# Optimization experiments

Measured on AMD Instinct MI355X. Metric: run time of the kernel, lower is better.

## Reference

```python
import jax, jax.numpy as jnp
import numpy as np

SR = 10  # self.sr in the torch module

def _linear_params(key, fan_in, fan_out):
    kw, kb = jax.random.split(key)
    bound = 1.0 / np.sqrt(fan_in)
    W = jax.random.uniform(kw, (fan_out, fan_in), jnp.float32, -bound, bound)
    b = jax.random.uniform(kb, (fan_out,), jnp.float32, -bound, bound)
    return W, b

def setup_inputs() -> dict:
    key = jax.random.key(0)
    ks = jax.random.split(key, 6)
    P, H = 2048, 1024
    R = C = P * SR
    X = jax.random.normal(ks[0], (R, C), jnp.float32)
    p = jax.random.randint(ks[1], (P,), 0, 64, jnp.int32)
    W1, b1 = _linear_params(ks[2], 1, H)
    W2, b2 = _linear_params(ks[3], H, H)
    W3, b3 = _linear_params(ks[4], H, H)
    W4, b4 = _linear_params(ks[5], H, 1)
    return {"X": X, "p": p, "W1": W1, "b1": b1, "W2": W2, "b2": b2,
            "W3": W3, "b3": b3, "W4": W4, "b4": b4}

def _forward(X, p, W1, b1, W2, b2, W3, b3, W4, b4):
    P = p.shape[0]
    C = X.shape[1]
    # shift_rows: only rows i*SR for i in [0, P-2] are populated; all other
    # rows of the shifted matrix are NaN and contribute 0 sum / 0 count below.
    rows = X[jnp.arange(P - 1) * SR]                      # (P-1, C)
    shifts = p[: P - 1]
    # torch.roll(x, s): out[j] = x[(j - s) mod C]
    cols = (jnp.arange(C)[None, :] - shifts[:, None]) % C  # (P-1, C)
    shifted = jnp.take_along_axis(rows, cols, axis=1)      # (P-1, C)
    # nan_mean over rows (NaN rows of the full matrix drop out identically)
    mask = jnp.isnan(shifted)
    col_sum = jnp.where(mask, 0.0, shifted).sum(axis=0)
    col_cnt = (~mask).sum(axis=0).astype(jnp.float32)
    m = jnp.where(col_cnt > 0, col_sum / col_cnt, jnp.float32(jnp.nan))  # (C,)
    # fill_nan_with_last_value: serial forward-fill (index 0 kept as-is)
    def step(last, xi):
        v = jnp.where(jnp.isnan(xi), last, xi)
        return v, v
    _, rest = jax.lax.scan(step, m[0], m[1:])
    filled = jnp.concatenate([m[:1], rest])                # (C,)
    x = filled[::SR][:P][:, None]                          # (P, 1)
    h = jax.nn.relu(x @ W1.T + b1)
    h = jax.nn.relu(h @ W2.T + b2)
    h = jax.nn.relu(h @ W3.T + b3)
    y = h @ W4.T + b4                                      # (P, 1)
    return y[:, 0]

def reference(X, p, W1, b1, W2, b2, W3, b3, W4, b4):
    return _forward(X, p, W1, b1, W2, b2, W3, b3, W4, b4)
```

## Files before the change

### kernel.cpp

```cpp
#include <hip/hip_runtime.h>
#include <hip/hip_bf16.h>

#define CC 20480
#define PP 2048
#define NROWS 2047
#define SRR 10
#define HH 1024
#define NCH 64

typedef __attribute__((ext_vector_type(8))) short short8;
typedef __attribute__((ext_vector_type(4))) float f32x4;

__device__ __forceinline__ void split_bf16(float v, unsigned short& hi, unsigned short& lo) {
    __hip_bfloat16 h = __float2bfloat16(v);
    float r = v - __bfloat162float(h);
    __hip_bfloat16 l2 = __float2bfloat16(r);
    hi = *(unsigned short*)&h;
    lo = *(unsigned short*)&l2;
}

__global__ __launch_bounds__(256) void pre_k(const float* __restrict__ X,
                                             const int* __restrict__ p,
                                             float* __restrict__ psum,
                                             const float* __restrict__ W2,
                                             unsigned short* __restrict__ w2h,
                                             unsigned short* __restrict__ w2l,
                                             const float* __restrict__ W3,
                                             unsigned short* __restrict__ w3h,
                                             unsigned short* __restrict__ w3l) {
    int b = blockIdx.x, t = threadIdx.x;
    if (b < 512) {
        int k = (b & 7) * 256 + t;
        int chunk = b >> 3;
        int r0 = chunk * 32;
        int r1 = r0 + 32; if (r1 > NROWS) r1 = NROWS;
        float s = 0.f;
        int base = SRR * k;
        for (int i = r0; i < r1; ++i) {
            int col = base - p[i]; if (col < 0) col += CC;
            s += X[(size_t)i * (size_t)(SRR * CC) + col];
        }
        psum[chunk * PP + k] = s;
        return;
    }
    int bb = b - 512;
    const float* src; unsigned short *dh, *dl;
    if (bb < 256) { src = W2; dh = w2h; dl = w2l; }
    else { src = W3; dh = w3h; dl = w3l; bb -= 256; }
    int idx = bb * 4096 + t * 16;
    #pragma unroll
    for (int q = 0; q < 4; ++q) {
        float4 v = *(const float4*)&src[idx + q * 4];
        float vv[4] = {v.x, v.y, v.z, v.w};
        ushort hi4[4], lo4[4];
        #pragma unroll
        for (int i = 0; i < 4; ++i) split_bf16(vv[i], hi4[i], lo4[i]);
        *(ushort4*)&dh[idx + q * 4] = *(ushort4*)hi4;
        *(ushort4*)&dl[idx + q * 4] = *(ushort4*)lo4;
    }
}

__device__ __forceinline__ void gload16(const unsigned short* g, unsigned short* lds) {
    __builtin_amdgcn_global_load_lds(
        (const __attribute__((address_space(1))) void*)g,
        (__attribute__((address_space(3))) void*)lds,
        16, 0, 0);
}

#define BM 128
#define BN 64
#define BK 32

__global__ __launch_bounds__(512, 2) void gemm1_k(
    const float* __restrict__ psum,
    const float* __restrict__ W1, const float* __restrict__ b1,
    const unsigned short* __restrict__ Bh, const unsigned short* __restrict__ Bl,
    const float* __restrict__ b2,
    unsigned short* __restrict__ Ch, unsigned short* __restrict__ Cl)
{
    __shared__ unsigned short Bb[2][4096];
    __shared__ float w1f[1024], b1f[1024], xv[128];

    int lin = blockIdx.x;
    int v = (lin & 7) * 32 + (lin >> 3);
    int bx = v >> 4, by = v & 15;
    int bm = bx * BM, bn = by * BN;
    int t = threadIdx.x, w = t >> 6, l = t & 63;
    int lr = l & 15, lk = l >> 4;
    int wr = w >> 1, wc = w & 1;

    size_t offB = (size_t)(bn + (w & 3) * 16 + lr) * HH + lk * 8;
#define BSTAGE(buf, k0)                                                      \
    do {                                                                     \
        if (w < 4) gload16(Bh + offB + (k0), Bb[buf] + w * 512);             \
        else       gload16(Bl + offB + (k0), Bb[buf] + 2048 + (w - 4) * 512);\
    } while (0)

    BSTAGE(0, 0);
    {
        int row = t >> 2, q = t & 3;
        float s = 0.f;
        #pragma unroll
        for (int j = 0; j < 16; ++j) s += psum[(q * 16 + j) * PP + bm + row];
        s += __shfl_xor(s, 1, 64);
        s += __shfl_xor(s, 2, 64);
        if (q == 0) xv[row] = s * (1.0f / (float)NROWS);
        if (t < 256) *(float4*)&w1f[t * 4] = *(const float4*)&W1[t * 4];
        else *(float4*)&b1f[(t - 256) * 4] = *(const float4*)&b1[(t - 256) * 4];
    }
    __syncthreads();

    float x0 = xv[wr * 32 + lr], x1 = xv[wr * 32 + 16 + lr];

    f32x4 acc[2][2];
    #pragma unroll
    for (int i = 0; i < 2; ++i)
        #pragma unroll
        for (int j = 0; j < 2; ++j) acc[i][j] = (f32x4)(0.f);

    int nt = HH / BK;
    for (int tt = 0; tt < nt; ++tt) {
        int cur = tt & 1;
        if (tt + 1 < nt) {
            BSTAGE(cur ^ 1, (tt + 1) * BK);
            asm volatile("s_waitcnt vmcnt(1)" ::: "memory");
        } else {
            asm volatile("s_waitcnt vmcnt(0)" ::: "memory");
        }
        __builtin_amdgcn_s_barrier();
        __builtin_amdgcn_sched_barrier(0);
        __builtin_amdgcn_s_setprio(1);
        int k0 = tt * BK;
        float4 wva = *(const float4*)&w1f[k0 + lk * 8];
        float4 wvb = *(const float4*)&w1f[k0 + lk * 8 + 4];
        float4 bva = *(const float4*)&b1f[k0 + lk * 8];
        float4 bvb = *(const float4*)&b1f[k0 + lk * 8 + 4];
        float wv[8] = {wva.x, wva.y, wva.z, wva.w, wvb.x, wvb.y, wvb.z, wvb.w};
        float bv2[8] = {bva.x, bva.y, bva.z, bva.w, bvb.x, bvb.y, bvb.z, bvb.w};
        ushort ahh[2][8], all2[2][8];
        #pragma unroll
        for (int mi = 0; mi < 2; ++mi) {
            float xm = mi ? x1 : x0;
            #pragma unroll
            for (int j = 0; j < 8; ++j) {
                float h = fmaf(xm, wv[j], bv2[j]);
                h = h > 0.f ? h : 0.f;
                split_bf16(h, ahh[mi][j], all2[mi][j]);
            }
        }
        short8 bh2[2], bl2[2];
        #pragma unroll
        for (int ni = 0; ni < 2; ++ni) {
            bh2[ni] = *(const short8*)&Bb[cur][(wc * 2 + ni) * 512 + l * 8];
            bl2[ni] = *(const short8*)&Bb[cur][2048 + (wc * 2 + ni) * 512 + l * 8];
        }
        #pragma unroll
        for (int mi = 0; mi < 2; ++mi) {
            short8 ah2 = *(short8*)ahh[mi];
            short8 al2 = *(short8*)all2[mi];
            #pragma unroll
            for (int ni = 0; ni < 2; ++ni) {
                acc[mi][ni] = __builtin_amdgcn_mfma_f32_16x16x32_bf16(ah2, bh2[ni], acc[mi][ni], 0, 0, 0);
                acc[mi][ni] = __builtin_amdgcn_mfma_f32_16x16x32_bf16(ah2, bl2[ni], acc[mi][ni], 0, 0, 0);
                acc[mi][ni] = __builtin_amdgcn_mfma_f32_16x16x32_bf16(al2, bh2[ni], acc[mi][ni], 0, 0, 0);
            }
        }
        __builtin_amdgcn_s_setprio(0);
        __builtin_amdgcn_sched_barrier(0);
        __builtin_amdgcn_s_barrier();
        __builtin_amdgcn_sched_barrier(0);
    }
#undef BSTAGE

    float bv[2];
    #pragma unroll
    for (int ni = 0; ni < 2; ++ni) bv[ni] = b2[bn + wc * 32 + ni * 16 + lr];
    #pragma unroll
    for (int mi = 0; mi < 2; ++mi)
        #pragma unroll
        for (int ni = 0; ni < 2; ++ni)
            #pragma unroll
            for (int r = 0; r < 4; ++r) {
                int row = bm + wr * 32 + mi * 16 + lk * 4 + r;
                int col = bn + wc * 32 + ni * 16 + lr;
                float vv = acc[mi][ni][r] + bv[ni];
                vv = vv > 0.f ? vv : 0.f;
                unsigned short hi, lo;
                split_bf16(vv, hi, lo);
                Ch[(size_t)row * HH + col] = hi;
                Cl[(size_t)row * HH + col] = lo;
            }
}

__global__ __launch_bounds__(512, 2) void gemm2_k(
    const unsigned short* __restrict__ Ah, const unsigned short* __restrict__ Al,
    const unsigned short* __restrict__ Bh, const unsigned short* __restrict__ Bl,
    const float* __restrict__ b3,
    const float* __restrict__ W4, float* __restrict__ partial)
{
    __shared__ unsigned short lds[2][12288];
    int lin = blockIdx.x;
    int v = (lin & 7) * 32 + (lin >> 3);
    int bx = v >> 4, by = v & 15;
    int bm = bx * BM, bn = by * BN;
    int t = threadIdx.x, w = t >> 6, l = t & 63;
    int lr = l & 15, lk = l >> 4;
    int wr = w >> 1, wc = w & 1;

    size_t offA = (size_t)(bm + w * 16 + lr) * HH + lk * 8;
    size_t offB = (size_t)(bn + (w & 3) * 16 + lr) * HH + lk * 8;

#define STAGE(buf, k0)                                                   \
    do {                                                                 \
        unsigned short* L = lds[buf];                                    \
        gload16(Ah + offA + (k0), L + w * 512);                          \
        gload16(Al + offA + (k0), L + 4096 + w * 512);                   \
        if (w < 4) gload16(Bh + offB + (k0), L + 8192 + w * 512);        \
        else       gload16(Bl + offB + (k0), L + 10240 + (w - 4) * 512); \
    } while (0)

    f32x4 acc[2][2];
    #pragma unroll
    for (int i = 0; i < 2; ++i)
        #pragma unroll
        for (int j = 0; j < 2; ++j) acc[i][j] = (f32x4)(0.f);

    STAGE(0, 0);

    int nt = HH / BK;
    for (int tt = 0; tt < nt; ++tt) {
        int cur = tt & 1;
        if (tt + 1 < nt) {
            STAGE(cur ^ 1, (tt + 1) * BK);
            asm volatile("s_waitcnt vmcnt(3)" ::: "memory");
        } else {
            asm volatile("s_waitcnt vmcnt(0)" ::: "memory");
        }
        __builtin_amdgcn_s_barrier();
        __builtin_amdgcn_sched_barrier(0);
        __builtin_amdgcn_s_setprio(1);
        unsigned short* L = lds[cur];
        short8 ah2[2], al2[2], bh2[2], bl2[2];
        #pragma unroll
        for (int mi = 0; mi < 2; ++mi) {
            ah2[mi] = *(const short8*)&L[(wr * 2 + mi) * 512 + l * 8];
            al2[mi] = *(const short8*)&L[4096 + (wr * 2 + mi) * 512 + l * 8];
        }
        #pragma unroll
        for (int ni = 0; ni < 2; ++ni) {
            bh2[ni] = *(const short8*)&L[8192 + (wc * 2 + ni) * 512 + l * 8];
            bl2[ni] = *(const short8*)&L[10240 + (wc * 2 + ni) * 512 + l * 8];
        }
        #pragma unroll
        for (int mi = 0; mi < 2; ++mi)
            #pragma unroll
            for (int ni = 0; ni < 2; ++ni) {
                acc[mi][ni] = __builtin_amdgcn_mfma_f32_16x16x32_bf16(ah2[mi], bh2[ni], acc[mi][ni], 0, 0, 0);
                acc[mi][ni] = __builtin_amdgcn_mfma_f32_16x16x32_bf16(ah2[mi], bl2[ni], acc[mi][ni], 0, 0, 0);
                acc[mi][ni] = __builtin_amdgcn_mfma_f32_16x16x32_bf16(al2[mi], bh2[ni], acc[mi][ni], 0, 0, 0);
            }
        __builtin_amdgcn_s_setprio(0);
        __builtin_amdgcn_sched_barrier(0);
        __builtin_amdgcn_s_barrier();
        __builtin_amdgcn_sched_barrier(0);
    }
#undef STAGE

    float bv[2], w4v[2];
    #pragma unroll
    for (int ni = 0; ni < 2; ++ni) {
        bv[ni]  = b3[bn + wc * 32 + ni * 16 + lr];
        w4v[ni] = W4[bn + wc * 32 + ni * 16 + lr];
    }
    #pragma unroll
    for (int mi = 0; mi < 2; ++mi) {
        float ps[4];
        #pragma unroll
        for (int r = 0; r < 4; ++r) {
            float acc_d = 0.f;
            #pragma unroll
            for (int ni = 0; ni < 2; ++ni) {
                float vv = acc[mi][ni][r] + bv[ni];
                vv = vv > 0.f ? vv : 0.f;
                acc_d += vv * w4v[ni];
            }
            ps[r] = acc_d;
        }
        #pragma unroll
        for (int r = 0; r < 4; ++r) {
            #pragma unroll
            for (int m2 = 1; m2 < 16; m2 <<= 1) ps[r] += __shfl_xor(ps[r], m2, 64);
        }
        if (lr == 0) {
            #pragma unroll
            for (int r = 0; r < 4; ++r) {
                int row = bm + wr * 32 + mi * 16 + lk * 4 + r;
                partial[(size_t)row * 32 + by * 2 + wc] = ps[r];
            }
        }
    }
}

__global__ __launch_bounds__(256) void ysum_k(const float* __restrict__ partial,
                                              const float* __restrict__ b4,
                                              float* __restrict__ y) {
    int r = blockIdx.x * 256 + threadIdx.x;
    float s = 0.f;
    #pragma unroll
    for (int q = 0; q < 8; ++q) {
        float4 v = *(const float4*)&partial[(size_t)r * 32 + q * 4];
        s += v.x + v.y + v.z + v.w;
    }
    y[r] = s + b4[0];
}

extern "C" void kernel_launch(void* const* d_in, const int* in_sizes, int n_in,
                              void* d_out, int out_size, void* d_ws, size_t ws_size,
                              hipStream_t stream) {
    const float* X  = (const float*)d_in[0];
    const int*   p  = (const int*)d_in[1];
    const float* W1 = (const float*)d_in[2];
    const float* b1 = (const float*)d_in[3];
    const float* W2 = (const float*)d_in[4];
    const float* b2 = (const float*)d_in[5];
    const float* W3 = (const float*)d_in[6];
    const float* b3 = (const float*)d_in[7];
    const float* W4 = (const float*)d_in[8];
    const float* b4 = (const float*)d_in[9];
    float* out = (float*)d_out;

    char* ws = (char*)d_ws;
    size_t off = 0;
    float* psum = (float*)(ws + off); off += (size_t)NCH * PP * 4;
    unsigned short* h2h = (unsigned short*)(ws + off); off += (size_t)PP * HH * 2;
    unsigned short* h2l = (unsigned short*)(ws + off); off += (size_t)PP * HH * 2;
    unsigned short* w2h = (unsigned short*)(ws + off); off += (size_t)HH * HH * 2;
    unsigned short* w2l = (unsigned short*)(ws + off); off += (size_t)HH * HH * 2;
    unsigned short* w3h = (unsigned short*)(ws + off); off += (size_t)HH * HH * 2;
    unsigned short* w3l = (unsigned short*)(ws + off); off += (size_t)HH * HH * 2;
    float* partial = (float*)(ws + off); off += (size_t)PP * 32 * 4;

    pre_k<<<1024, 256, 0, stream>>>(X, p, psum, W2, w2h, w2l, W3, w3h, w3l);
    gemm1_k<<<256, 512, 0, stream>>>(psum, W1, b1, w2h, w2l, b2, h2h, h2l);
    gemm2_k<<<256, 512, 0, stream>>>(h2h, h2l, w3h, w3l, b3, W4, partial);
    ysum_k<<<PP / 256, 256, 0, stream>>>(partial, b4, out);
}
```

Before: 83.97 us.

## Load A operands directly to registers in gemm2, keep only B in LDS

In the second GEMM kernel, the A hi/lo fragments are now loaded straight from global memory into registers, double-buffered across two register sets, instead of being staged through LDS. Only the B tiles still go through LDS double buffering, which shrinks LDS from 48KB to 16KB per block and removes the A-side LDS reads. The aim is to cut LDS traffic and footprint, possibly allowing more resident blocks. The cost is more registers for the A buffers and uncoalesced-ish direct global loads, with the waitcnt count adjusted to match.

```diff
diff --git a/kernel.cpp b/kernel.cpp
--- a/kernel.cpp
+++ b/kernel.cpp
@@ -198,7 +198,8 @@
     const float* __restrict__ b3,
     const float* __restrict__ W4, float* __restrict__ partial)
 {
-    __shared__ unsigned short lds[2][12288];
+    __shared__ unsigned short Bb[2][4096];
+
     int lin = blockIdx.x;
     int v = (lin & 7) * 32 + (lin >> 3);
     int bx = v >> 4, by = v & 15;
@@ -207,64 +208,75 @@
     int lr = l & 15, lk = l >> 4;
     int wr = w >> 1, wc = w & 1;
 
-    size_t offA = (size_t)(bm + w * 16 + lr) * HH + lk * 8;
+    const unsigned short* gAh = Ah + (size_t)(bm + wr * 32 + lr) * HH + lk * 8;
+    const unsigned short* gAl = Al + (size_t)(bm + wr * 32 + lr) * HH + lk * 8;
+
     size_t offB = (size_t)(bn + (w & 3) * 16 + lr) * HH + lk * 8;
-
-#define STAGE(buf, k0)                                                   \
-    do {                                                                 \
-        unsigned short* L = lds[buf];                                    \
-        gload16(Ah + offA + (k0), L + w * 512);                          \
-        gload16(Al + offA + (k0), L + 4096 + w * 512);                   \
-        if (w < 4) gload16(Bh + offB + (k0), L + 8192 + w * 512);        \
-        else       gload16(Bl + offB + (k0), L + 10240 + (w - 4) * 512); \
+#define BSTAGE(buf, k0)                                                      \
+    do {                                                                     \
+        if (w < 4) gload16(Bh + offB + (k0), Bb[buf] + w * 512);             \
+        else       gload16(Bl + offB + (k0), Bb[buf] + 2048 + (w - 4) * 512);\
     } while (0)
 
+#define ALOAD(dst, k0)                                            \
+    do {                                                          \
+        dst[0][0] = *(const short8*)(gAh + (k0));                 \
+        dst[0][1] = *(const short8*)(gAl + (k0));                 \
+        dst[1][0] = *(const short8*)(gAh + 16 * HH + (k0));       \
+        dst[1][1] = *(const short8*)(gAl + 16 * HH + (k0));       \
+    } while (0)
+
+    short8 aA[2][2], aB[2][2];
+    ALOAD(aA, 0);
+    BSTAGE(0, 0);
+    __syncthreads();
+
     f32x4 acc[2][2];
     #pragma unroll
     for (int i = 0; i < 2; ++i)
         #pragma unroll
         for (int j = 0; j < 2; ++j) acc[i][j] = (f32x4)(0.f);
 
-    STAGE(0, 0);
-
     int nt = HH / BK;
-    for (int tt = 0; tt < nt; ++tt) {
-        int cur = tt & 1;
-        if (tt + 1 < nt) {
-            STAGE(cur ^ 1, (tt + 1) * BK);
-            asm volatile("s_waitcnt vmcnt(3)" ::: "memory");
-        } else {
-            asm volatile("s_waitcnt vmcnt(0)" ::: "memory");
-        }
-        __builtin_amdgcn_s_barrier();
-        __builtin_amdgcn_sched_barrier(0);
-        __builtin_amdgcn_s_setprio(1);
-        unsigned short* L = lds[cur];
-        short8 ah2[2], al2[2], bh2[2], bl2[2];
-        #pragma unroll
-        for (int mi = 0; mi < 2; ++mi) {
-            ah2[mi] = *(const short8*)&L[(wr * 2 + mi) * 512 + l * 8];
-            al2[mi] = *(const short8*)&L[4096 + (wr * 2 + mi) * 512 + l * 8];
-        }
-        #pragma unroll
-        for (int ni = 0; ni < 2; ++ni) {
-            bh2[ni] = *(const short8*)&L[8192 + (wc * 2 + ni) * 512 + l * 8];
-            bl2[ni] = *(const short8*)&L[10240 + (wc * 2 + ni) * 512 + l * 8];
-        }
-        #pragma unroll
-        for (int mi = 0; mi < 2; ++mi)
-            #pragma unroll
-            for (int ni = 0; ni < 2; ++ni) {
-                acc[mi][ni] = __builtin_amdgcn_mfma_f32_16x16x32_bf16(ah2[mi], bh2[ni], acc[mi][ni], 0, 0, 0);
-                acc[mi][ni] = __builtin_amdgcn_mfma_f32_16x16x32_bf16(ah2[mi], bl2[ni], acc[mi][ni], 0, 0, 0);
-                acc[mi][ni] = __builtin_amdgcn_mfma_f32_16x16x32_bf16(al2[mi], bh2[ni], acc[mi][ni], 0, 0, 0);
-            }
-        __builtin_amdgcn_s_setprio(0);
-        __builtin_amdgcn_sched_barrier(0);
-        __builtin_amdgcn_s_barrier();
-        __builtin_amdgcn_sched_barrier(0);
-    }
-#undef STAGE
+#define G2BODY(TT, CUR, ACUR, ANXT)                                            \
+    do {                                                                       \
+        if ((TT) + 1 < nt) {                                                   \
+            ALOAD(ANXT, ((TT) + 1) * BK);             \
+            BSTAGE((CUR) ^ 1, ((TT) + 1) * BK);       \
+            asm volatile("s_waitcnt vmcnt(5)" ::: "memory");   \
+        } else {                                                               \
+            asm volatile("s_waitcnt vmcnt(0)" ::: "memory");                   \
+        }                                                                      \
+        __builtin_amdgcn_s_barrier();                                          \
+        __builtin_amdgcn_sched_barrier(0);                                     \
+        __builtin_amdgcn_s_setprio(1);                                         \
+        short8 bh2[2], bl2[2];                                                 \
+        _Pragma("unroll")                                                      \
+        for (int ni = 0; ni < 2; ++ni) {                                       \
+            bh2[ni] = *(const short8*)&Bb[CUR][(wc * 2 + ni) * 512 + l * 8];   \
+            bl2[ni] = *(const short8*)&Bb[CUR][2048 + (wc * 2 + ni) * 512 + l * 8];\
+        }                                                                      \
+        _Pragma("unroll")                                                      \
+        for (int mi = 0; mi < 2; ++mi)                                         \
+            _Pragma("unroll")                                                  \
+            for (int ni = 0; ni < 2; ++ni) {                                   \
+                acc[mi][ni] = __builtin_amdgcn_mfma_f32_16x16x32_bf16(ACUR[mi][0], bh2[ni], acc[mi][ni], 0, 0, 0); \
+                acc[mi][ni] = __builtin_amdgcn_mfma_f32_16x16x32_bf16(ACUR[mi][0], bl2[ni], acc[mi][ni], 0, 0, 0); \
+                acc[mi][ni] = __builtin_amdgcn_mfma_f32_16x16x32_bf16(ACUR[mi][1], bh2[ni], acc[mi][ni], 0, 0, 0); \
+            }                                                                  \
+        __builtin_amdgcn_s_setprio(0);                                         \
+        __builtin_amdgcn_sched_barrier(0);                                     \
+        __builtin_amdgcn_s_barrier();                                          \
+        __builtin_amdgcn_sched_barrier(0);                                     \
+    } while (0)
+
+    for (int tt = 0; tt < nt; tt += 2) {
+        G2BODY(tt,     0, aA, aB);
+        G2BODY(tt + 1, 1, aB, aA);
+    }
+#undef G2BODY
+#undef ALOAD
+#undef BSTAGE
 
     float bv[2], w4v[2];
     #pragma unroll
```

Measured after the change: 100.8 us. 1.2x slower.
